# Kernel tuning notes

Hardware: AMD Instinct MI355X
Metric: run time of the kernel (lower is better)

## Reference

```python
import jax, jax.numpy as jnp
import numpy as np

# dims: B batch, T timesteps, S sensors, O obs_dim, E obs_embed_dim, P pe_emb_dim, A inter-sensor attn dim
B, T, S, O, E, P, A, OUT = 64, 128, 64, 4, 64, 16, 10, 128


def positional_encoding(times, pe_dim):
    # standard sinusoidal PE over continuous times -> (B, T, pe_dim)
    # (sin block then cos block; mathematically same frequencies as interleaved torch version)
    freq = jnp.exp(jnp.arange(0, pe_dim, 2, dtype=jnp.float32) * (-jnp.log(10000.0) / pe_dim))
    ang = times[..., None] * freq  # (B, T, pe_dim//2)
    return jnp.concatenate([jnp.sin(ang), jnp.cos(ang)], axis=-1)


def setup_inputs() -> dict:
    key = jax.random.key(0)
    ks = jax.random.split(key, 16)
    x = jax.random.normal(ks[0], (B, T, S, O), dtype=jnp.float32)
    times = jnp.sort(jax.random.uniform(ks[1], (B, T), dtype=jnp.float32) * 100.0, axis=1)
    mask = (jax.random.uniform(ks[2], (B, T, S), dtype=jnp.float32) < 0.8).astype(jnp.float32)
    s = 0.1  # param scale (module inits near zero; use small random for a meaningful baseline)
    params = dict(
        obs_emb_weights=jax.random.normal(ks[3], (S, O, E), dtype=jnp.float32) * s,
        inter_sensor_attn_weights=jax.random.normal(ks[4], (S, A), dtype=jnp.float32) * s,
        W_recv=jax.random.normal(ks[5], (E, A + P), dtype=jnp.float32) * s,
        b_recv=jax.random.normal(ks[6], (A + P,), dtype=jnp.float32) * s,
        bidir_weights=jax.random.normal(ks[7], (S, E), dtype=jnp.float32) * s,
        W_q=jax.random.normal(ks[8], (E + P, A), dtype=jnp.float32) * s,
        b_q=jax.random.normal(ks[9], (A,), dtype=jnp.float32) * s,
        W_k=jax.random.normal(ks[10], (E + P, A), dtype=jnp.float32) * s,
        b_k=jax.random.normal(ks[11], (A,), dtype=jnp.float32) * s,
        W_s=jax.random.normal(ks[12], (T, 1), dtype=jnp.float32) * s,
        b_s=jax.random.normal(ks[13], (1,), dtype=jnp.float32) * s,
        W_emb=jax.random.normal(ks[14], (E + P, OUT), dtype=jnp.float32) * s,
        b_emb=jax.random.normal(ks[15], (OUT,), dtype=jnp.float32) * s,
    )
    return dict(x=x, times=times, mask=mask, **params)


def reference(x, times, mask, obs_emb_weights, inter_sensor_attn_weights,
              W_recv, b_recv, bidir_weights, W_q, b_q, W_k, b_k,
              W_s, b_s, W_emb, b_emb):
    b, t, s, _ = x.shape
    e = obs_emb_weights.shape[-1]
    pe_dim = W_recv.shape[1] - inter_sensor_attn_weights.shape[1]

    # per-sensor observation embedding, masked
    h = jax.nn.relu(jnp.einsum('btso,soe->btse', x, obs_emb_weights))
    h = h * mask[..., None]

    pe = positional_encoding(times, pe_dim)                      # (B,T,P)
    pe_rep = jnp.broadcast_to(pe[:, :, None, :], (b, t, s, pe_dim))

    # inter-sensor attention alpha: (B,T,S_recv,S_send)
    attn_cat = jnp.concatenate(
        [jnp.broadcast_to(inter_sensor_attn_weights[None, None], (b, t, s, inter_sensor_attn_weights.shape[1])),
         pe_rep], axis=-1)                                        # (B,T,S,A+P)
    h_map = h @ W_recv + b_recv                                   # (B,T,S,A+P)
    alpha = jax.nn.relu(jnp.einsum('btid,btjd->btij', h_map, attn_cat))

    bidir = bidir_weights @ bidir_weights.T                       # (S,S)

    def propagate(h_in, adj):
        # fused form of: (h.unsqueeze(2) * (bidir*alpha*adj)[...,None]).sum(3)
        w = bidir[None, None] * alpha * adj[:, None]              # (B,T,S,S)
        return jax.nn.relu(jnp.einsum('btij,btje->btie', w, h_in))

    adj1 = jnp.ones((b, s, s), dtype=x.dtype)
    h = propagate(h, adj1)
    adj2 = adj1 * (alpha.sum(axis=1) / mask.sum(axis=1)[..., None])  # (B,S,S)
    h = propagate(h, adj2)

    H = jnp.concatenate([h, pe_rep], axis=-1).transpose(0, 2, 1, 3)  # (B,S,T,E+P)

    # temporal self-attention
    Q = H @ W_q + b_q                                             # (B,S,T,A)
    K = H @ W_k + b_k
    scale = 1.0 / jnp.sqrt(jnp.float32(e + pe_dim))
    beta = jnp.einsum('bsta,bsua->bstu', Q, K) * scale            # (B,S,T,T)
    beta = (beta @ W_s)[..., 0] + b_s[0]                          # (B,S,T)
    beta = jax.nn.softmax(beta, axis=-1)

    out = jnp.einsum('bst,bstd->bsd', beta, H) @ W_emb + b_emb    # (B,S,OUT)
    return out
```

## Files before the change

kernel.cpp:

```cpp
#include <hip/hip_runtime.h>
#include <hip/hip_bf16.h>


typedef unsigned short u16;
typedef unsigned int u32;
typedef __attribute__((ext_vector_type(8))) short short8;
typedef __attribute__((ext_vector_type(4))) float f32x4;

#define OFF_PE    0
#define OFF_BIDIR 131072
#define OFF_MS    135168
#define OFF_ADJ   139264
#define OFF_BRP   401408
#define OFF_ST    401424
#define BOFF_WRT  1638464u
#define BOFF_CATX 1642560u
#define BOFF_PEH  1644608u
#define BOFF_ADJS 1906752u
#define BOFF_V    2431040u
#define BOFF_HH   3479616u

__device__ __forceinline__ u16 f2bf(float f){
  __hip_bfloat16 h = __float2bfloat16(f);
  union { __hip_bfloat16 h; u16 u; } v; v.h = h; return v.u;
}
__device__ __forceinline__ u32 pk2bf(float lo, float hi){
  __hip_bfloat162 h = __float22bfloat162_rn(float2{lo, hi});
  union { __hip_bfloat162 h; u32 u; } v; v.h = h; return v.u;
}
__device__ __forceinline__ float bf2f(u16 h){
  union { u32 u; float f; } v; v.u = ((u32)h) << 16; return v.f;
}

__global__ void k_pre(const float* __restrict__ times, const float* __restrict__ mask,
                      const float* __restrict__ Wb, const float* __restrict__ Wrecv,
                      const float* __restrict__ brecv, const float* __restrict__ battn,
                      float* __restrict__ ws_f, char* __restrict__ ws_b) {
  __shared__ float peL[32][17];
  __shared__ float wpe[64][17];
  __shared__ float pm[4][64];
  const int blk = blockIdx.x, tid = threadIdx.x;
  u16* wrt  = (u16*)(ws_b + BOFF_WRT);
  u16* catx = (u16*)(ws_b + BOFF_CATX);
  u16* peh  = (u16*)(ws_b + BOFF_PEH);
  u16* vv   = (u16*)(ws_b + BOFF_V);
  float* ST = ws_f + OFF_ST;
  if (blk < 256) {
    float* PE = ws_f + OFF_PE;
    #pragma unroll
    for (int r = 0; r < 2; ++r) {
      int id = blk * 512 + r * 256 + tid;
      int bt = id >> 4, k = id & 15;
      float tv = times[bt];
      int kk = k & 7;
      float fr = expf(-(float)kk * 1.1512925465f);
      float ang = tv * fr;
      float v = (k < 8) ? sinf(ang) : cosf(ang);
      PE[id] = v;
      peh[id] = f2bf(v);
      peL[r*16 + (tid >> 4)][k] = v;
    }
    #pragma unroll
    for (int q = 0; q < 4; ++q) {
      int idx = q * 256 + tid;
      wpe[idx >> 4][idx & 15] = Wrecv[(idx >> 4)*26 + 10 + (idx & 15)];
    }
    __syncthreads();
    {
      int btl = tid >> 3, e0 = (tid & 7) * 8;
      float acc[8];
      #pragma unroll
      for (int i = 0; i < 8; ++i) acc[i] = 0.f;
      #pragma unroll
      for (int k = 0; k < 16; ++k) {
        float p = peL[btl][k];
        #pragma unroll
        for (int i = 0; i < 8; ++i) acc[i] += wpe[e0 + i][k] * p;
      }
      u32* dst = (u32*)&vv[(blk*32 + btl)*64 + e0];
      #pragma unroll
      for (int p = 0; p < 4; ++p) dst[p] = pk2bf(acc[2*p], acc[2*p+1]);
      if (tid < 32) {
        float s = 0.f;
        #pragma unroll
        for (int k = 0; k < 16; ++k) s += brecv[10 + k] * peL[tid][k];
        ST[blk*32 + tid] = s;
      }
    }
  } else if (blk < 260) {
    float* bidir = ws_f + OFF_BIDIR;
    int q = blk - 256;
    for (int rr = 0; rr < 4; ++rr) {
      int idx = (q*4 + rr) * 256 + tid;
      int i = idx >> 6, j = idx & 63;
      float acc = 0.f;
      for (int e = 0; e < 64; ++e) acc += Wb[i*64+e] * Wb[j*64+e];
      bidir[idx] = acc;
    }
  } else if (blk == 260) {
    for (int r = 0; r < 8; ++r) {
      int idx = r * 256 + tid;
      int d = idx >> 6, e = idx & 63;
      wrt[idx] = (d < 26) ? f2bf(Wrecv[e*26 + d]) : (u16)0;
    }
    if (tid < 16) ws_f[OFF_BRP + tid] = (tid < 10) ? brecv[tid] : 0.f;
    #pragma unroll
    for (int i = 0; i < 4; ++i) {
      int idx = i * 256 + tid;
      int j = idx >> 4, d = idx & 15;
      catx[idx] = (d < 10) ? f2bf(battn[j*10 + d]) : ((d == 10) ? f2bf(1.f) : (u16)0);
    }
  } else {
    int b = blk - 261;
    int i = tid & 63, q = tid >> 6;
    float s = 0.f;
    for (int t = q*32; t < q*32 + 32; ++t) s += mask[(b*128 + t)*64 + i];
    pm[q][i] = s;
    __syncthreads();
    if (tid < 64)
      (ws_f + OFF_MS)[b*64 + tid] = pm[0][tid] + pm[1][tid] + pm[2][tid] + pm[3][tid];
  }
}

__global__ __launch_bounds__(256)
void k_adj(const float* __restrict__ x, const float* __restrict__ mask,
           const float* __restrict__ Wobs, float* __restrict__ ws_f,
           const char* __restrict__ ws_b) {
  __shared__ __align__(16) u16 hA[64][72];
  __shared__ __align__(16) u16 hmA[64][24];

  const int tid = threadIdx.x;
  const int b = blockIdx.y, tc = blockIdx.x;
  const int w = tid >> 6, l = tid & 63, lr = l & 15, lq = l >> 4, kb = lq * 8;
  const u16* wrt  = (const u16*)(ws_b + BOFF_WRT);
  const u16* catx = (const u16*)(ws_b + BOFF_CATX);
  const u16* vv   = (const u16*)(ws_b + BOFF_V);
  const float* brp = ws_f + OFF_BRP;
  const float* ST = ws_f + OFF_ST;
  float* adj = ws_f + OFF_ADJ;

  const short8 z8 = (short8){0,0,0,0,0,0,0,0};
  const bool lowk = (lq < 2);
  short8 w0 = z8, w1 = z8;
  if (lr < 10) {
    const u16* wr = wrt + lr * 64;
    w0 = *(const short8*)&wr[kb];
    w1 = *(const short8*)&wr[32 + kb];
  }
  short8 bc[4];
  #pragma unroll
  for (int n = 0; n < 4; ++n)
    bc[n] = lowk ? *(const short8*)&catx[(16*n + lr)*16 + lq*8] : z8;
  float4 bv = *(const float4*)&brp[lq*4];

  f32x4 asum[4];
  #pragma unroll
  for (int n = 0; n < 4; ++n) asum[n] = (f32x4){0.f,0.f,0.f,0.f};

  const int e4 = tid & 15, sg = tid >> 4;

  for (int tt = 0; tt < 8; ++tt) {
    int t = tc * 8 + tt;
    int base = b * 128 + t;
    short8 av0 = z8, av1 = z8;
    if (lr == 10) {
      av0 = *(const short8*)&vv[base*64 + kb];
      av1 = *(const short8*)&vv[base*64 + 32 + kb];
    }
    float st = ST[base];
    {
      float4 mk4 = *(const float4*)&mask[base*64 + sg*4];
      float mks[4] = {mk4.x, mk4.y, mk4.z, mk4.w};
      #pragma unroll
      for (int si = 0; si < 4; ++si) {
        int s = sg*4 + si;
        float4 xv = *(const float4*)&x[base*256 + s*4];
        float xo[4] = {xv.x, xv.y, xv.z, xv.w};
        float ax = 0.f, ay = 0.f, az = 0.f, aw = 0.f;
        #pragma unroll
        for (int o = 0; o < 4; ++o) {
          float4 wv = *(const float4*)&Wobs[(s*4+o)*64 + e4*4];
          ax += xo[o]*wv.x; ay += xo[o]*wv.y; az += xo[o]*wv.z; aw += xo[o]*wv.w;
        }
        float mk = mks[si];
        uint2 p;
        p.x = pk2bf(fmaxf(ax,0.f)*mk, fmaxf(ay,0.f)*mk);
        p.y = pk2bf(fmaxf(az,0.f)*mk, fmaxf(aw,0.f)*mk);
        *(uint2*)&hA[s][e4*4] = p;
      }
    }
    __syncthreads();
    {
      short8 a0 = (lr < 10) ? w0 : av0;
      short8 a1 = (lr < 10) ? w1 : av1;
      f32x4 acc = (f32x4){0.f,0.f,0.f,0.f};
      short8 b0 = *(const short8*)&hA[16*w + lr][kb];
      short8 b1 = *(const short8*)&hA[16*w + lr][32 + kb];
      acc = __builtin_amdgcn_mfma_f32_16x16x32_bf16(a0, b0, acc, 0, 0, 0);
      acc = __builtin_amdgcn_mfma_f32_16x16x32_bf16(a1, b1, acc, 0, 0, 0);
      uint2 qq;
      qq.x = pk2bf(acc[0]+bv.x, acc[1]+bv.y);
      qq.y = pk2bf(acc[2]+bv.z, acc[3]+bv.w);
      *(uint2*)&hmA[16*w + lr][lq*4] = qq;
    }
    __syncthreads();
    {
      short8 am = lowk ? *(const short8*)&hmA[16*w + lr][lq*8] : z8;
      #pragma unroll
      for (int n = 0; n < 4; ++n) {
        f32x4 z = (f32x4){st, st, st, st};
        z = __builtin_amdgcn_mfma_f32_16x16x32_bf16(am, bc[n], z, 0, 0, 0);
        #pragma unroll
        for (int reg = 0; reg < 4; ++reg) asum[n][reg] += fmaxf(z[reg], 0.f);
      }
    }
    __syncthreads();
  }
  #pragma unroll
  for (int n = 0; n < 4; ++n) {
    #pragma unroll
    for (int reg = 0; reg < 4; ++reg) {
      int i = 16*w + lq*4 + reg, j = 16*n + lr;
      atomicAdd(&adj[((size_t)b << 12) + (i << 6) + j], asum[n][reg]);
    }
  }
}

__global__ __launch_bounds__(256)
void k_scale(const float* __restrict__ ws_f, char* __restrict__ ws_b) {
  const int b = blockIdx.x, tid = threadIdx.x;
  const float* adj = ws_f + OFF_ADJ + (size_t)b * 4096;
  const float* ms = ws_f + OFF_MS + b * 64;
  u16* as_ = (u16*)(ws_b + BOFF_ADJS) + (size_t)b * 4096;
  #pragma unroll
  for (int k = 0; k < 16; ++k) {
    int idx = k * 256 + tid;
    int i = idx >> 6;
    as_[idx] = f2bf(adj[idx] / ms[i]);
  }
}

__global__ __launch_bounds__(256, 4)
void k_main(const float* __restrict__ x, const float* __restrict__ mask,
            const float* __restrict__ Wobs, const float* __restrict__ ws_f,
            const char* __restrict__ ws_b, u16* __restrict__ Hh) {
  __shared__ __align__(16) char smem[36864];
  u16 (*hA)[72]  = (u16 (*)[72])(smem);
  u16 (*hT)[72]  = (u16 (*)[72])(smem + 9216);
  u16 (*wA)[72]  = (u16 (*)[72])(smem + 18432);
  u16 (*hmA)[24] = (u16 (*)[24])(smem + 27648);
  u16 (*adjS)[72]= (u16 (*)[72])(smem + 27648);

  const int tid = threadIdx.x;
  const int t = blockIdx.x, b = blockIdx.y;
  const int w = tid >> 6, l = tid & 63, lr = l & 15, lq = l >> 4, kb = lq * 8;
  const int base = b * 128 + t;
  const u16* wrt  = (const u16*)(ws_b + BOFF_WRT);
  const u16* catx = (const u16*)(ws_b + BOFF_CATX);
  const u16* vv   = (const u16*)(ws_b + BOFF_V);
  const float* bidirG = ws_f + OFF_BIDIR;
  const float* brp = ws_f + OFF_BRP;
  const int i0 = 16*w + lq*4;
  const short8 z8 = (short8){0,0,0,0,0,0,0,0};
  const bool lowk = (lq < 2);

  const uint4* ag = (const uint4*)(ws_b + BOFF_ADJS + (size_t)b * 8192);
  uint4 g0 = ag[2*tid], g1 = ag[2*tid + 1];
  short8 w0 = z8, w1 = z8;
  if (lr < 10) {
    const u16* wr = wrt + lr * 64;
    w0 = *(const short8*)&wr[kb];
    w1 = *(const short8*)&wr[32 + kb];
  }
  short8 av0 = z8, av1 = z8;
  if (lr == 10) {
    av0 = *(const short8*)&vv[base*64 + kb];
    av1 = *(const short8*)&vv[base*64 + 32 + kb];
  }
  short8 bc[4];
  #pragma unroll
  for (int n = 0; n < 4; ++n)
    bc[n] = lowk ? *(const short8*)&catx[(16*n + lr)*16 + lq*8] : z8;
  float4 bv = *(const float4*)&brp[lq*4];
  const float st = (ws_f + OFF_ST)[base];

  {
    const int e4 = tid & 15, sg = tid >> 4;
    float4 mk4 = *(const float4*)&mask[base*64 + sg*4];
    float mks[4] = {mk4.x, mk4.y, mk4.z, mk4.w};
    #pragma unroll
    for (int si = 0; si < 4; ++si) {
      int s = sg*4 + si;
      float4 xv = *(const float4*)&x[base*256 + s*4];
      float xo[4] = {xv.x, xv.y, xv.z, xv.w};
      float ax = 0.f, ay = 0.f, az = 0.f, aw = 0.f;
      #pragma unroll
      for (int o = 0; o < 4; ++o) {
        float4 wv = *(const float4*)&Wobs[(s*4+o)*64 + e4*4];
        ax += xo[o]*wv.x; ay += xo[o]*wv.y; az += xo[o]*wv.z; aw += xo[o]*wv.w;
      }
      float mk = mks[si];
      uint2 p;
      p.x = pk2bf(fmaxf(ax,0.f)*mk, fmaxf(ay,0.f)*mk);
      p.y = pk2bf(fmaxf(az,0.f)*mk, fmaxf(aw,0.f)*mk);
      *(uint2*)&hA[s][e4*4] = p;
    }
  }
  __syncthreads();

  {
    #pragma unroll
    for (int sp = 0; sp < 8; ++sp) {
      int s = w*16 + sp*2;
      *(u32*)&hT[l][s] = (u32)hA[s][l] | ((u32)hA[s+1][l] << 16);
    }
    short8 a0 = (lr < 10) ? w0 : av0;
    short8 a1 = (lr < 10) ? w1 : av1;
    f32x4 acc = (f32x4){0.f,0.f,0.f,0.f};
    short8 b0 = *(const short8*)&hA[16*w + lr][kb];
    short8 b1 = *(const short8*)&hA[16*w + lr][32 + kb];
    acc = __builtin_amdgcn_mfma_f32_16x16x32_bf16(a0, b0, acc, 0, 0, 0);
    acc = __builtin_amdgcn_mfma_f32_16x16x32_bf16(a1, b1, acc, 0, 0, 0);
    uint2 qq;
    qq.x = pk2bf(acc[0]+bv.x, acc[1]+bv.y);
    qq.y = pk2bf(acc[2]+bv.z, acc[3]+bv.w);
    *(uint2*)&hmA[16*w + lr][lq*4] = qq;
  }
  __syncthreads();

  {
    short8 am = lowk ? *(const short8*)&hmA[16*w + lr][lq*8] : z8;
    #pragma unroll
    for (int n = 0; n < 4; ++n) {
      f32x4 z = (f32x4){st, st, st, st};
      z = __builtin_amdgcn_mfma_f32_16x16x32_bf16(am, bc[n], z, 0, 0, 0);
      int j = 16*n + lr;
      #pragma unroll
      for (int reg = 0; reg < 4; ++reg) {
        float w1v = fmaxf(z[reg], 0.f) * bidirG[((i0+reg) << 6) + j];
        wA[i0 + reg][j] = f2bf(w1v);
      }
    }
  }
  __syncthreads();

  {
    int idx0 = 2*tid, idx1 = 2*tid + 1;
    *(uint4*)&adjS[idx0 >> 3][(idx0 & 7) * 8] = g0;
    *(uint4*)&adjS[idx1 >> 3][(idx1 & 7) * 8] = g1;

    short8 aw0 = *(const short8*)&wA[16*w + lr][kb];
    short8 aw1 = *(const short8*)&wA[16*w + lr][32 + kb];
    #pragma unroll
    for (int n = 0; n < 4; ++n) {
      f32x4 acc = (f32x4){0.f,0.f,0.f,0.f};
      short8 b0 = *(const short8*)&hT[16*n + lr][kb];
      short8 b1 = *(const short8*)&hT[16*n + lr][32 + kb];
      acc = __builtin_amdgcn_mfma_f32_16x16x32_bf16(aw0, b0, acc, 0, 0, 0);
      acc = __builtin_amdgcn_mfma_f32_16x16x32_bf16(aw1, b1, acc, 0, 0, 0);
      int e = 16*n + lr;
      uint2 pp;
      pp.x = pk2bf(fmaxf(acc[0],0.f), fmaxf(acc[1],0.f));
      pp.y = pk2bf(fmaxf(acc[2],0.f), fmaxf(acc[3],0.f));
      *(uint2*)&hA[e][i0] = pp;
    }
  }
  __syncthreads();

  {
    int row = 16*w + lr;
    union { short8 v; u16 h[8]; u32 u[4]; } uw0, uw1, ud0, ud1, oa, ob;
    uw0.v = *(const short8*)&wA[row][kb];
    uw1.v = *(const short8*)&wA[row][32 + kb];
    ud0.v = *(const short8*)&adjS[row][kb];
    ud1.v = *(const short8*)&adjS[row][32 + kb];
    #pragma unroll
    for (int k = 0; k < 4; ++k) {
      oa.u[k] = pk2bf(bf2f(uw0.h[2*k])*bf2f(ud0.h[2*k]),
                      bf2f(uw0.h[2*k+1])*bf2f(ud0.h[2*k+1]));
      ob.u[k] = pk2bf(bf2f(uw1.h[2*k])*bf2f(ud1.h[2*k]),
                      bf2f(uw1.h[2*k+1])*bf2f(ud1.h[2*k+1]));
    }
    short8 a20 = oa.v, a21 = ob.v;
    size_t obase = ((size_t)b * 64) * 8192 + (size_t)t * 64;
    #pragma unroll
    for (int n = 0; n < 4; ++n) {
      f32x4 acc = (f32x4){0.f,0.f,0.f,0.f};
      short8 b0 = *(const short8*)&hA[16*n + lr][kb];
      short8 b1 = *(const short8*)&hA[16*n + lr][32 + kb];
      acc = __builtin_amdgcn_mfma_f32_16x16x32_bf16(a20, b0, acc, 0, 0, 0);
      acc = __builtin_amdgcn_mfma_f32_16x16x32_bf16(a21, b1, acc, 0, 0, 0);
      int e = 16*n + lr;
      u32 p0 = pk2bf(fmaxf(acc[0],0.f), fmaxf(acc[1],0.f));
      u32 p1 = pk2bf(fmaxf(acc[2],0.f), fmaxf(acc[3],0.f));
      Hh[obase + (size_t)(i0+0) * 8192 + e] = (u16)p0;
      Hh[obase + (size_t)(i0+1) * 8192 + e] = (u16)(p0 >> 16);
      Hh[obase + (size_t)(i0+2) * 8192 + e] = (u16)p1;
      Hh[obase + (size_t)(i0+3) * 8192 + e] = (u16)(p1 >> 16);
    }
  }
}

#define HTP 82
#define PEP 17

__global__ __launch_bounds__(512)
void k_attn(const float* __restrict__ ws_f, const u16* __restrict__ Hh,
            const float* __restrict__ Wq, const float* __restrict__ bq,
            const float* __restrict__ Wk, const float* __restrict__ bk,
            const float* __restrict__ Ws, const float* __restrict__ bs,
            const float* __restrict__ Wemb, const float* __restrict__ bemb,
            float* __restrict__ out) {
  __shared__ u16 Ht[128][HTP];
  __shared__ float peB[128][PEP];
  __shared__ float wsL[128];
  __shared__ float pA[6][80];
  __shared__ float pK[8][10];
  __shared__ float qvL[80];
  __shared__ float pC[4][128];
  __shared__ float bb[128];
  __shared__ float red[4];
  __shared__ float cstL, sWL;

  const int tid = threadIdx.x;
  const int s = blockIdx.x, b = blockIdx.y;
  const float scale = 0.111803398875f;

  const u16* src = Hh + ((size_t)b * 64 + s) * 8192;
  #pragma unroll
  for (int r = 0; r < 2; ++r) {
    int id = r * 512 + tid;
    int tt = id >> 3, c = (id & 7) * 8;
    uint4 q = *(const uint4*)&src[tt * 64 + c];
    u32* dst = (u32*)&Ht[tt][c];
    dst[0] = q.x; dst[1] = q.y; dst[2] = q.z; dst[3] = q.w;
  }
  #pragma unroll
  for (int r = 0; r < 4; ++r) {
    int id = r * 512 + tid;
    peB[id >> 4][id & 15] = ws_f[OFF_PE + (size_t)b * 2048 + id];
  }
  if (tid < 128) wsL[tid] = Ws[tid];
  __syncthreads();

  if (tid < 480) {
    int d = tid % 80, c = tid / 80;
    int t0 = c * 22, t1 = (t0 + 22 > 128) ? 128 : t0 + 22;
    float a0 = 0.f, a1 = 0.f, a2 = 0.f, a3 = 0.f;
    int t = t0;
    if (d < 64) {
      for (; t + 4 <= t1; t += 4) {
        a0 += wsL[t]   * bf2f(Ht[t][d]);
        a1 += wsL[t+1] * bf2f(Ht[t+1][d]);
        a2 += wsL[t+2] * bf2f(Ht[t+2][d]);
        a3 += wsL[t+3] * bf2f(Ht[t+3][d]);
      }
      for (; t < t1; ++t) a0 += wsL[t] * bf2f(Ht[t][d]);
    } else {
      int k = d - 64;
      for (; t + 4 <= t1; t += 4) {
        a0 += wsL[t]   * peB[t][k];
        a1 += wsL[t+1] * peB[t+1][k];
        a2 += wsL[t+2] * peB[t+2][k];
        a3 += wsL[t+3] * peB[t+3][k];
      }
      for (; t < t1; ++t) a0 += wsL[t] * peB[t][k];
    }
    pA[c][d] = (a0 + a1) + (a2 + a3);
  } else if (tid == 480) {
    float a0 = 0.f, a1 = 0.f, a2 = 0.f, a3 = 0.f;
    for (int t = 0; t < 128; t += 4) {
      a0 += wsL[t]; a1 += wsL[t+1]; a2 += wsL[t+2]; a3 += wsL[t+3];
    }
    sWL = (a0 + a1) + (a2 + a3);
  }
  __syncthreads();

  if (tid < 80) {
    int a = tid % 10, c = tid / 10;
    float a0 = 0.f, a1 = 0.f;
    #pragma unroll
    for (int i = 0; i < 10; i += 2) {
      int d = c * 10 + i;
      float h0 = pA[0][d] + pA[1][d] + pA[2][d] + pA[3][d] + pA[4][d] + pA[5][d];
      float h1 = pA[0][d+1] + pA[1][d+1] + pA[2][d+1] + pA[3][d+1] + pA[4][d+1] + pA[5][d+1];
      a0 += h0 * Wk[d * 10 + a];
      a1 += h1 * Wk[(d+1) * 10 + a];
    }
    pK[c][a] = a0 + a1;
  }
  __syncthreads();

  if (tid <= 80) {
    float kt[10];
    #pragma unroll
    for (int a = 0; a < 10; ++a) {
      float acc = sWL * bk[a];
      #pragma unroll
      for (int c = 0; c < 8; ++c) acc += pK[c][a];
      kt[a] = acc;
    }
    if (tid < 80) {
      float a0 = 0.f, a1 = 0.f;
      #pragma unroll
      for (int a = 0; a < 10; a += 2) {
        a0 += Wq[tid * 10 + a] * kt[a];
        a1 += Wq[tid * 10 + a + 1] * kt[a + 1];
      }
      qvL[tid] = a0 + a1;
    } else {
      float cq = 0.f;
      #pragma unroll
      for (int a = 0; a < 10; ++a) cq += bq[a] * kt[a];
      cstL = scale * cq + bs[0];
    }
  }
  __syncthreads();

  {
    int t = tid & 127, q = tid >> 7;
    float a0 = 0.f, a1 = 0.f, a2 = 0.f, a3 = 0.f;
    const u32* row = (const u32*)&Ht[t][0];
    if (q == 0) {
      #pragma unroll
      for (int i = 0; i < 10; i += 2) {
        u32 p0 = row[i], p1 = row[i+1];
        a0 += bf2f((u16)p0) * qvL[2*i]   + bf2f((u16)(p0 >> 16)) * qvL[2*i+1];
        a1 += bf2f((u16)p1) * qvL[2*i+2] + bf2f((u16)(p1 >> 16)) * qvL[2*i+3];
      }
    } else if (q == 1) {
      #pragma unroll
      for (int i = 10; i < 20; i += 2) {
        u32 p0 = row[i], p1 = row[i+1];
        a0 += bf2f((u16)p0) * qvL[2*i]   + bf2f((u16)(p0 >> 16)) * qvL[2*i+1];
        a1 += bf2f((u16)p1) * qvL[2*i+2] + bf2f((u16)(p1 >> 16)) * qvL[2*i+3];
      }
    } else if (q == 2) {
      #pragma unroll
      for (int i = 20; i < 32; i += 4) {
        u32 p0 = row[i], p1 = row[i+1], p2 = row[i+2], p3 = row[i+3];
        a0 += bf2f((u16)p0) * qvL[2*i]   + bf2f((u16)(p0 >> 16)) * qvL[2*i+1];
        a1 += bf2f((u16)p1) * qvL[2*i+2] + bf2f((u16)(p1 >> 16)) * qvL[2*i+3];
        a2 += bf2f((u16)p2) * qvL[2*i+4] + bf2f((u16)(p2 >> 16)) * qvL[2*i+5];
        a3 += bf2f((u16)p3) * qvL[2*i+6] + bf2f((u16)(p3 >> 16)) * qvL[2*i+7];
      }
    } else {
      #pragma unroll
      for (int k = 0; k < 16; k += 4) {
        a0 += peB[t][k]   * qvL[64 + k];
        a1 += peB[t][k+1] * qvL[65 + k];
        a2 += peB[t][k+2] * qvL[66 + k];
        a3 += peB[t][k+3] * qvL[67 + k];
      }
    }
    pC[q][t] = (a0 + a1) + (a2 + a3);
  }
  __syncthreads();

  if (tid < 128) {
    float v = scale * (pC[0][tid] + pC[1][tid] + pC[2][tid] + pC[3][tid]) + cstL;
    bb[tid] = v;
    float mm = v;
    #pragma unroll
    for (int off = 32; off; off >>= 1) mm = fmaxf(mm, __shfl_xor(mm, off));
    if ((tid & 63) == 0) red[tid >> 6] = mm;
  }
  __syncthreads();
  float mx = fmaxf(red[0], red[1]);
  if (tid < 128) {
    float ev = expf(bb[tid] - mx);
    bb[tid] = ev;
    float ss = ev;
    #pragma unroll
    for (int off = 32; off; off >>= 1) ss += __shfl_xor(ss, off);
    if ((tid & 63) == 0) red[2 + (tid >> 6)] = ss;
  }
  __syncthreads();

  if (tid < 480) {
    int d = tid % 80, c = tid / 80;
    int t0 = c * 22, t1 = (t0 + 22 > 128) ? 128 : t0 + 22;
    float a0 = 0.f, a1 = 0.f, a2 = 0.f, a3 = 0.f;
    int t = t0;
    if (d < 64) {
      for (; t + 4 <= t1; t += 4) {
        a0 += bb[t]   * bf2f(Ht[t][d]);
        a1 += bb[t+1] * bf2f(Ht[t+1][d]);
        a2 += bb[t+2] * bf2f(Ht[t+2][d]);
        a3 += bb[t+3] * bf2f(Ht[t+3][d]);
      }
      for (; t < t1; ++t) a0 += bb[t] * bf2f(Ht[t][d]);
    } else {
      int k = d - 64;
      for (; t + 4 <= t1; t += 4) {
        a0 += bb[t]   * peB[t][k];
        a1 += bb[t+1] * peB[t+1][k];
        a2 += bb[t+2] * peB[t+2][k];
        a3 += bb[t+3] * peB[t+3][k];
      }
      for (; t < t1; ++t) a0 += bb[t] * peB[t][k];
    }
    pA[c][d] = (a0 + a1) + (a2 + a3);
  }
  __syncthreads();

  {
    int o = tid & 127, q = tid >> 7;
    int d0 = q * 20;
    float a0 = 0.f, a1 = 0.f, a2 = 0.f, a3 = 0.f;
    #pragma unroll
    for (int i = 0; i < 20; i += 4) {
      int d = d0 + i;
      float h0 = pA[0][d]   + pA[1][d]   + pA[2][d]   + pA[3][d]   + pA[4][d]   + pA[5][d];
      float h1 = pA[0][d+1] + pA[1][d+1] + pA[2][d+1] + pA[3][d+1] + pA[4][d+1] + pA[5][d+1];
      float h2 = pA[0][d+2] + pA[1][d+2] + pA[2][d+2] + pA[3][d+2] + pA[4][d+2] + pA[5][d+2];
      float h3 = pA[0][d+3] + pA[1][d+3] + pA[2][d+3] + pA[3][d+3] + pA[4][d+3] + pA[5][d+3];
      a0 += h0 * Wemb[d * 128 + o];
      a1 += h1 * Wemb[(d+1) * 128 + o];
      a2 += h2 * Wemb[(d+2) * 128 + o];
      a3 += h3 * Wemb[(d+3) * 128 + o];
    }
    pC[q][o] = (a0 + a1) + (a2 + a3);
  }
  __syncthreads();
  if (tid < 128) {
    float rdenom = 1.0f / (red[2] + red[3]);
    out[(((size_t)b * 64 + s) << 7) + tid] =
        bemb[tid] + (pC[0][tid] + pC[1][tid] + pC[2][tid] + pC[3][tid]) * rdenom;
  }
}

extern "C" void kernel_launch(void* const* d_in, const int* in_sizes, int n_in,
                              void* d_out, int out_size, void* d_ws, size_t ws_size,
                              hipStream_t stream) {
  (void)in_sizes; (void)n_in; (void)out_size; (void)ws_size;
  const float* x     = (const float*)d_in[0];
  const float* times = (const float*)d_in[1];
  const float* mask  = (const float*)d_in[2];
  const float* Wobs  = (const float*)d_in[3];
  const float* Wattn = (const float*)d_in[4];
  const float* Wrecv = (const float*)d_in[5];
  const float* brecv = (const float*)d_in[6];
  const float* Wb    = (const float*)d_in[7];
  const float* Wq    = (const float*)d_in[8];
  const float* bq    = (const float*)d_in[9];
  const float* Wk    = (const float*)d_in[10];
  const float* bk    = (const float*)d_in[11];
  const float* Ws    = (const float*)d_in[12];
  const float* bs    = (const float*)d_in[13];
  const float* Wemb  = (const float*)d_in[14];
  const float* bemb  = (const float*)d_in[15];
  float* out = (float*)d_out;
  float* ws_f = (float*)d_ws;
  char* ws_b = (char*)d_ws;
  u16* Hh = (u16*)(ws_b + BOFF_HH);

  hipMemsetAsync(ws_b + (size_t)OFF_ADJ * 4, 0, (size_t)64 * 64 * 64 * 4, stream);
  k_pre<<<325, 256, 0, stream>>>(times, mask, Wb, Wrecv, brecv, Wattn, ws_f, ws_b);
  k_adj<<<dim3(16, 64), 256, 0, stream>>>(x, mask, Wobs, ws_f, ws_b);
  k_scale<<<64, 256, 0, stream>>>(ws_f, ws_b);
  k_main<<<dim3(128, 64), 256, 0, stream>>>(x, mask, Wobs, ws_f, ws_b, Hh);
  k_attn<<<dim3(64, 64), 512, 0, stream>>>(ws_f, Hh, Wq, bq, Wk, bk, Ws, bs, Wemb, bemb, out);
}
```

Before: 150.9 us.

## Fold adjacency scaling into main kernel, stage H output via LDS, use bf16 PE

Removes the separate k_scale launch. k_main now reads the fp32 adjacency sums directly and scales them by a precomputed reciprocal of the mask sums (k_pre now stores 1/msum). The second-propagation output is staged in shared memory and written to global as coalesced 16-byte rows instead of scattered 2-byte stores. k_attn loads the bf16 positional encoding instead of the fp32 copy, so the fp32 PE write is dropped. In exchange, each k_main block reads 16KB of fp32 adjacency instead of 8KB of bf16, and the PE loses precision.

```diff
diff --git a/kernel.cpp b/kernel.cpp
--- a/kernel.cpp
+++ b/kernel.cpp
@@ -16,7 +16,6 @@
 #define BOFF_WRT  1638464u
 #define BOFF_CATX 1642560u
 #define BOFF_PEH  1644608u
-#define BOFF_ADJS 1906752u
 #define BOFF_V    2431040u
 #define BOFF_HH   3479616u
 
@@ -46,7 +45,6 @@
   u16* vv   = (u16*)(ws_b + BOFF_V);
   float* ST = ws_f + OFF_ST;
   if (blk < 256) {
-    float* PE = ws_f + OFF_PE;
     #pragma unroll
     for (int r = 0; r < 2; ++r) {
       int id = blk * 512 + r * 256 + tid;
@@ -56,7 +54,6 @@
       float fr = expf(-(float)kk * 1.1512925465f);
       float ang = tv * fr;
       float v = (k < 8) ? sinf(ang) : cosf(ang);
-      PE[id] = v;
       peh[id] = f2bf(v);
       peL[r*16 + (tid >> 4)][k] = v;
     }
@@ -118,7 +115,8 @@
     pm[q][i] = s;
     __syncthreads();
     if (tid < 64)
-      (ws_f + OFF_MS)[b*64 + tid] = pm[0][tid] + pm[1][tid] + pm[2][tid] + pm[3][tid];
+      (ws_f + OFF_MS)[b*64 + tid] =
+          1.0f / (pm[0][tid] + pm[1][tid] + pm[2][tid] + pm[3][tid]);
   }
 }
 
@@ -226,20 +224,6 @@
   }
 }
 
-__global__ __launch_bounds__(256)
-void k_scale(const float* __restrict__ ws_f, char* __restrict__ ws_b) {
-  const int b = blockIdx.x, tid = threadIdx.x;
-  const float* adj = ws_f + OFF_ADJ + (size_t)b * 4096;
-  const float* ms = ws_f + OFF_MS + b * 64;
-  u16* as_ = (u16*)(ws_b + BOFF_ADJS) + (size_t)b * 4096;
-  #pragma unroll
-  for (int k = 0; k < 16; ++k) {
-    int idx = k * 256 + tid;
-    int i = idx >> 6;
-    as_[idx] = f2bf(adj[idx] / ms[i]);
-  }
-}
-
 __global__ __launch_bounds__(256, 4)
 void k_main(const float* __restrict__ x, const float* __restrict__ mask,
             const float* __restrict__ Wobs, const float* __restrict__ ws_f,
@@ -250,6 +234,7 @@
   u16 (*wA)[72]  = (u16 (*)[72])(smem + 18432);
   u16 (*hmA)[24] = (u16 (*)[24])(smem + 27648);
   u16 (*adjS)[72]= (u16 (*)[72])(smem + 27648);
+  u16 (*h2L)[72] = (u16 (*)[72])(smem + 9216);
 
   const int tid = threadIdx.x;
   const int t = blockIdx.x, b = blockIdx.y;
@@ -260,12 +245,15 @@
   const u16* vv   = (const u16*)(ws_b + BOFF_V);
   const float* bidirG = ws_f + OFF_BIDIR;
   const float* brp = ws_f + OFF_BRP;
+  const float* msInv = ws_f + OFF_MS + b * 64;
   const int i0 = 16*w + lq*4;
   const short8 z8 = (short8){0,0,0,0,0,0,0,0};
   const bool lowk = (lq < 2);
 
-  const uint4* ag = (const uint4*)(ws_b + BOFF_ADJS + (size_t)b * 8192);
-  uint4 g0 = ag[2*tid], g1 = ag[2*tid + 1];
+  const float4* agf = (const float4*)(ws_f + OFF_ADJ + (size_t)b * 4096);
+  float4 ga0 = agf[tid], ga1 = agf[tid + 256], ga2 = agf[tid + 512], ga3 = agf[tid + 768];
+  float msr0 = msInv[(tid >> 4)], msr1 = msInv[(tid >> 4) + 16],
+        msr2 = msInv[(tid >> 4) + 32], msr3 = msInv[(tid >> 4) + 48];
   short8 w0 = z8, w1 = z8;
   if (lr < 10) {
     const u16* wr = wrt + lr * 64;
@@ -345,9 +333,16 @@
   __syncthreads();
 
   {
-    int idx0 = 2*tid, idx1 = 2*tid + 1;
-    *(uint4*)&adjS[idx0 >> 3][(idx0 & 7) * 8] = g0;
-    *(uint4*)&adjS[idx1 >> 3][(idx1 & 7) * 8] = g1;
+    int arow = tid >> 4, acol = (tid & 15) * 4;
+    uint2 p;
+    p.x = pk2bf(ga0.x*msr0, ga0.y*msr0); p.y = pk2bf(ga0.z*msr0, ga0.w*msr0);
+    *(uint2*)&adjS[arow][acol] = p;
+    p.x = pk2bf(ga1.x*msr1, ga1.y*msr1); p.y = pk2bf(ga1.z*msr1, ga1.w*msr1);
+    *(uint2*)&adjS[arow + 16][acol] = p;
+    p.x = pk2bf(ga2.x*msr2, ga2.y*msr2); p.y = pk2bf(ga2.z*msr2, ga2.w*msr2);
+    *(uint2*)&adjS[arow + 32][acol] = p;
+    p.x = pk2bf(ga3.x*msr3, ga3.y*msr3); p.y = pk2bf(ga3.z*msr3, ga3.w*msr3);
+    *(uint2*)&adjS[arow + 48][acol] = p;
 
     short8 aw0 = *(const short8*)&wA[16*w + lr][kb];
     short8 aw1 = *(const short8*)&wA[16*w + lr][32 + kb];
@@ -382,7 +377,6 @@
                       bf2f(uw1.h[2*k+1])*bf2f(ud1.h[2*k+1]));
     }
     short8 a20 = oa.v, a21 = ob.v;
-    size_t obase = ((size_t)b * 64) * 8192 + (size_t)t * 64;
     #pragma unroll
     for (int n = 0; n < 4; ++n) {
       f32x4 acc = (f32x4){0.f,0.f,0.f,0.f};
@@ -393,26 +387,35 @@
       int e = 16*n + lr;
       u32 p0 = pk2bf(fmaxf(acc[0],0.f), fmaxf(acc[1],0.f));
       u32 p1 = pk2bf(fmaxf(acc[2],0.f), fmaxf(acc[3],0.f));
-      Hh[obase + (size_t)(i0+0) * 8192 + e] = (u16)p0;
-      Hh[obase + (size_t)(i0+1) * 8192 + e] = (u16)(p0 >> 16);
-      Hh[obase + (size_t)(i0+2) * 8192 + e] = (u16)p1;
-      Hh[obase + (size_t)(i0+3) * 8192 + e] = (u16)(p1 >> 16);
-    }
+      h2L[i0+0][e] = (u16)p0;
+      h2L[i0+1][e] = (u16)(p0 >> 16);
+      h2L[i0+2][e] = (u16)p1;
+      h2L[i0+3][e] = (u16)(p1 >> 16);
+    }
+  }
+  __syncthreads();
+
+  {
+    int i = tid >> 2, q = tid & 3;
+    const uint4* srcv = (const uint4*)&h2L[i][q * 16];
+    uint4 v0 = srcv[0], v1 = srcv[1];
+    size_t obase = ((size_t)b * 64) * 8192 + (size_t)t * 64;
+    uint4* dst = (uint4*)&Hh[obase + (size_t)i * 8192 + q * 16];
+    dst[0] = v0; dst[1] = v1;
   }
 }
 
 #define HTP 82
-#define PEP 17
 
 __global__ __launch_bounds__(512)
-void k_attn(const float* __restrict__ ws_f, const u16* __restrict__ Hh,
+void k_attn(const char* __restrict__ ws_b, const u16* __restrict__ Hh,
             const float* __restrict__ Wq, const float* __restrict__ bq,
             const float* __restrict__ Wk, const float* __restrict__ bk,
             const float* __restrict__ Ws, const float* __restrict__ bs,
             const float* __restrict__ Wemb, const float* __restrict__ bemb,
             float* __restrict__ out) {
   __shared__ u16 Ht[128][HTP];
-  __shared__ float peB[128][PEP];
+  __shared__ u16 peB[128][18];
   __shared__ float wsL[128];
   __shared__ float pA[6][80];
   __shared__ float pK[8][10];
@@ -425,6 +428,7 @@
   const int tid = threadIdx.x;
   const int s = blockIdx.x, b = blockIdx.y;
   const float scale = 0.111803398875f;
+  const u16* peh = (const u16*)(ws_b + BOFF_PEH);
 
   const u16* src = Hh + ((size_t)b * 64 + s) * 8192;
   #pragma unroll
@@ -436,9 +440,10 @@
     dst[0] = q.x; dst[1] = q.y; dst[2] = q.z; dst[3] = q.w;
   }
   #pragma unroll
-  for (int r = 0; r < 4; ++r) {
+  for (int r = 0; r < 2; ++r) {
     int id = r * 512 + tid;
-    peB[id >> 4][id & 15] = ws_f[OFF_PE + (size_t)b * 2048 + id];
+    u32 pv = ((const u32*)(peh + (size_t)b * 2048))[id];
+    *(u32*)&peB[id >> 3][(id & 7) * 2] = pv;
   }
   if (tid < 128) wsL[tid] = Ws[tid];
   __syncthreads();
@@ -459,12 +464,12 @@
     } else {
       int k = d - 64;
       for (; t + 4 <= t1; t += 4) {
-        a0 += wsL[t]   * peB[t][k];
-        a1 += wsL[t+1] * peB[t+1][k];
-        a2 += wsL[t+2] * peB[t+2][k];
-        a3 += wsL[t+3] * peB[t+3][k];
-      }
-      for (; t < t1; ++t) a0 += wsL[t] * peB[t][k];
+        a0 += wsL[t]   * bf2f(peB[t][k]);
+        a1 += wsL[t+1] * bf2f(peB[t+1][k]);
+        a2 += wsL[t+2] * bf2f(peB[t+2][k]);
+        a3 += wsL[t+3] * bf2f(peB[t+3][k]);
+      }
+      for (; t < t1; ++t) a0 += wsL[t] * bf2f(peB[t][k]);
     }
     pA[c][d] = (a0 + a1) + (a2 + a3);
   } else if (tid == 480) {
@@ -547,10 +552,10 @@
     } else {
       #pragma unroll
       for (int k = 0; k < 16; k += 4) {
-        a0 += peB[t][k]   * qvL[64 + k];
-        a1 += peB[t][k+1] * qvL[65 + k];
-        a2 += peB[t][k+2] * qvL[66 + k];
-        a3 += peB[t][k+3] * qvL[67 + k];
+        a0 += bf2f(peB[t][k])   * qvL[64 + k];
+        a1 += bf2f(peB[t][k+1]) * qvL[65 + k];
+        a2 += bf2f(peB[t][k+2]) * qvL[66 + k];
+        a3 += bf2f(peB[t][k+3]) * qvL[67 + k];
       }
     }
     pC[q][t] = (a0 + a1) + (a2 + a3);
@@ -593,12 +598,12 @@
     } else {
       int k = d - 64;
       for (; t + 4 <= t1; t += 4) {
-        a0 += bb[t]   * peB[t][k];
-        a1 += bb[t+1] * peB[t+1][k];
-        a2 += bb[t+2] * peB[t+2][k];
-        a3 += bb[t+3] * peB[t+3][k];
-      }
-      for (; t < t1; ++t) a0 += bb[t] * peB[t][k];
+        a0 += bb[t]   * bf2f(peB[t][k]);
+        a1 += bb[t+1] * bf2f(peB[t+1][k]);
+        a2 += bb[t+2] * bf2f(peB[t+2][k]);
+        a3 += bb[t+3] * bf2f(peB[t+3][k]);
+      }
+      for (; t < t1; ++t) a0 += bb[t] * bf2f(peB[t][k]);
     }
     pA[c][d] = (a0 + a1) + (a2 + a3);
   }
@@ -658,7 +663,6 @@
   hipMemsetAsync(ws_b + (size_t)OFF_ADJ * 4, 0, (size_t)64 * 64 * 64 * 4, stream);
   k_pre<<<325, 256, 0, stream>>>(times, mask, Wb, Wrecv, brecv, Wattn, ws_f, ws_b);
   k_adj<<<dim3(16, 64), 256, 0, stream>>>(x, mask, Wobs, ws_f, ws_b);
-  k_scale<<<64, 256, 0, stream>>>(ws_f, ws_b);
   k_main<<<dim3(128, 64), 256, 0, stream>>>(x, mask, Wobs, ws_f, ws_b, Hh);
-  k_attn<<<dim3(64, 64), 512, 0, stream>>>(ws_f, Hh, Wq, bq, Wk, bk, Ws, bs, Wemb, bemb, out);
-}
+  k_attn<<<dim3(64, 64), 512, 0, stream>>>(ws_b, Hh, Wq, bq, Wk, bk, Ws, bs, Wemb, bemb, out);
+}
```

Measured after the change: 161.3 us. 6.9% more time.
